# Performance work log

Hardware: AMD Instinct MI355X
Metric: run time of the kernel (lower is better)

## Reference

```python
import jax, jax.numpy as jnp
import numpy as np

B, E, H, C, R = 16, 1024, 1024, 64, 64  # batch, input_size, hidden_size, context_size, context_rank
H4 = 4 * H


def setup_inputs() -> dict:
    key = jax.random.key(0)
    ks = jax.random.split(key, 12)
    n = lambda k, shape, scale: jax.random.normal(k, shape, dtype=jnp.float32) * scale
    return {
        'x': n(ks[0], (B, E), 1.0),
        'h': n(ks[1], (B, H), 1.0),
        'c': n(ks[2], (B, H), 1.0),
        'context': n(ks[3], (B, C), 1.0),
        'Wi': n(ks[4], (E, H4), 0.02),
        'Wi_b': n(ks[5], (H4,), 0.02),
        'Wh': n(ks[6], (H, H4), 0.02),
        'Wh_b': n(ks[7], (H4,), 0.02),
        'AZ_il': n(ks[8], (C, E, R), 0.02),
        'AZ_ir': n(ks[9], (R, H4, C), 0.02),
        'AZ_hl': n(ks[10], (C, H, R), 0.02),
        'AZ_hr': n(ks[11], (R, H4, C), 0.02),
    }


def reference(x, h, c, context, Wi, Wi_b, Wh, Wh_b, AZ_il, AZ_ir, AZ_hl, AZ_hr):
    hs = Wh.shape[0]
    # compute_context_weights: per-sample low-rank weight perturbations
    lhs_i = jnp.einsum('bc,cer->ber', context, AZ_il)      # [B,E,R]
    rhs_i = jnp.einsum('bc,rjc->brj', context, AZ_ir)      # [B,R,4H]
    A_i = jnp.einsum('ber,brj->bej', lhs_i, rhs_i)         # [B,E,4H]
    lhs_h = jnp.einsum('bc,chr->bhr', context, AZ_hl)      # [B,H,R]
    rhs_h = jnp.einsum('bc,rjc->brj', context, AZ_hr)      # [B,R,4H]
    A_h = jnp.einsum('bhr,brj->bhj', lhs_h, rhs_h)         # [B,H,4H]
    # forward (faithful to original: context weights are multiplied by 0)
    Wi_eff = 0.0 * A_i + Wi                                # [B,E,4H]
    Wh_eff = 0.0 * A_h + Wh                                # [B,H,4H]
    ifgo = (jnp.einsum('be,bej->bj', x, Wi_eff) + Wi_b
            + jnp.einsum('bh,bhj->bj', h, Wh_eff) + Wh_b)  # [B,4H]
    i = jax.nn.sigmoid(ifgo[:, :hs])
    f = jax.nn.sigmoid(ifgo[:, hs:2 * hs])
    g = jnp.tanh(ifgo[:, 2 * hs:3 * hs])
    o = jax.nn.sigmoid(ifgo[:, 3 * hs:])
    c_new = f * c + i * g
    h_new = o * jnp.tanh(c_new)
    return (h_new, c_new)
```

## Files before the change

### kernel.cpp

```cpp
#include <hip/hip_runtime.h>
#include <stdint.h>

#define H4_ 4096
#define B_  16

__global__ __launch_bounds__(256) void k1_gemm(
    const float* __restrict__ x, const float* __restrict__ h,
    const float* __restrict__ Wi, const float* __restrict__ Wh,
    float* __restrict__ part)
{
    __shared__ float a_lds[256][16];
    __shared__ float red[8][16][32];

    const int s  = blockIdx.x & 7;
    const int ct = blockIdx.x >> 3;
    const int j0 = ct * 32;
    const int t  = threadIdx.x;
    const int c8 = t & 7;
    const int bq = (t >> 3) & 3;
    const int ks = t >> 5;

    float acc[4][4];
    #pragma unroll
    for (int r = 0; r < 4; r++)
        #pragma unroll
        for (int c = 0; c < 4; c++) acc[r][c] = 0.f;

    const float* A  = (s < 4) ? x : h;
    const float* W  = (s < 4) ? Wi : Wh;
    const int    e0 = (s & 3) * 256;

    {
        const int b = t & 15, kc = t >> 4;
        const float* src = A + b * 1024 + e0 + kc * 16;
        float4 v0 = *(const float4*)(src);
        float4 v1 = *(const float4*)(src + 4);
        float4 v2 = *(const float4*)(src + 8);
        float4 v3 = *(const float4*)(src + 12);
        const float vv[16] = { v0.x, v0.y, v0.z, v0.w, v1.x, v1.y, v1.z, v1.w,
                               v2.x, v2.y, v2.z, v2.w, v3.x, v3.y, v3.z, v3.w };
        #pragma unroll
        for (int j = 0; j < 16; j++) a_lds[kc * 16 + j][b] = vv[j];
    }
    __syncthreads();

    const float* wp = W + (size_t)e0 * H4_ + j0 + c8 * 4;
    #pragma unroll 8
    for (int i = 0; i < 32; i++) {
        const int kl = ks * 32 + i;
        float4 w = *(const float4*)(wp + (size_t)kl * H4_);
        float4 a = *(const float4*)&a_lds[kl][bq * 4];
        acc[0][0] += a.x * w.x; acc[0][1] += a.x * w.y; acc[0][2] += a.x * w.z; acc[0][3] += a.x * w.w;
        acc[1][0] += a.y * w.x; acc[1][1] += a.y * w.y; acc[1][2] += a.y * w.z; acc[1][3] += a.y * w.w;
        acc[2][0] += a.z * w.x; acc[2][1] += a.z * w.y; acc[2][2] += a.z * w.z; acc[2][3] += a.z * w.w;
        acc[3][0] += a.w * w.x; acc[3][1] += a.w * w.y; acc[3][2] += a.w * w.z; acc[3][3] += a.w * w.w;
    }

    #pragma unroll
    for (int r = 0; r < 4; r++)
        *(float4*)&red[ks][bq * 4 + r][c8 * 4] =
            make_float4(acc[r][0], acc[r][1], acc[r][2], acc[r][3]);
    __syncthreads();
    {
        const int b = t >> 4, c = t & 15;
        float s0 = 0.f, s1 = 0.f;
        #pragma unroll
        for (int kk = 0; kk < 8; kk++) {
            s0 += red[kk][b][c];
            s1 += red[kk][b][c + 16];
        }
        float* dst = part + ((size_t)s * B_ + b) * H4_ + j0;
        dst[c]      = s0;
        dst[c + 16] = s1;
    }
}

__global__ __launch_bounds__(256) void k2_act(
    const float* __restrict__ part, const float* __restrict__ c,
    const float* __restrict__ Wi_b, const float* __restrict__ Wh_b,
    float* __restrict__ out)
{
    const int tg = blockIdx.x * 256 + threadIdx.x;
    const int b  = tg >> 10;
    const int j  = tg & 1023;

    float g4[4];
    #pragma unroll
    for (int g = 0; g < 4; g++) {
        const int col = g * 1024 + j;
        float acc = Wi_b[col] + Wh_b[col];
        #pragma unroll
        for (int ss = 0; ss < 8; ss++)
            acc += part[((size_t)ss * B_ + b) * H4_ + col];
        g4[g] = acc;
    }
    const float ig = 1.f / (1.f + __expf(-g4[0]));
    const float fg = 1.f / (1.f + __expf(-g4[1]));
    const float gg = tanhf(g4[2]);
    const float og = 1.f / (1.f + __expf(-g4[3]));
    const float cv = c[tg];
    const float cn = fg * cv + ig * gg;
    const float hn = og * tanhf(cn);
    out[tg]         = hn;
    out[16384 + tg] = cn;
}

__global__ __launch_bounds__(256) void k_fused2(
    const float* __restrict__ x, const float* __restrict__ h,
    const float* __restrict__ cin,
    const float* __restrict__ Wi, const float* __restrict__ Wh,
    const float* __restrict__ Wi_b, const float* __restrict__ Wh_b,
    float* __restrict__ out)
{
    __shared__ float a_lds[256][16];
    __shared__ float red[16][16][16];
    __shared__ float gsum[16][16];

    const int bl = blockIdx.x;
    const int j0 = (bl & 7) * 128 + (bl >> 3) * 4;
    const int t  = threadIdx.x;
    const int g  = t & 3;
    const int bq = (t >> 2) & 3;
    const int ks = t >> 4;

    float acc[4][4];
    #pragma unroll
    for (int r = 0; r < 4; r++)
        #pragma unroll
        for (int c = 0; c < 4; c++) acc[r][c] = 0.f;

    for (int m = 0; m < 8; ++m) {
        const float* A  = (m < 4) ? x : h;
        const float* W  = (m < 4) ? Wi : Wh;
        const int    e0 = (m & 3) * 256;
        {
            const int b = t & 15, kc = t >> 4;
            const float* src = A + b * 1024 + e0 + kc * 16;
            float4 v0 = *(const float4*)(src);
            float4 v1 = *(const float4*)(src + 4);
            float4 v2 = *(const float4*)(src + 8);
            float4 v3 = *(const float4*)(src + 12);
            const float vv[16] = { v0.x, v0.y, v0.z, v0.w, v1.x, v1.y, v1.z, v1.w,
                                   v2.x, v2.y, v2.z, v2.w, v3.x, v3.y, v3.z, v3.w };
            #pragma unroll
            for (int jj = 0; jj < 16; jj++) a_lds[kc * 16 + jj][b] = vv[jj];
        }
        __syncthreads();
        const float* wp = W + (size_t)e0 * H4_ + g * 1024 + j0;
        #pragma unroll 4
        for (int i = 0; i < 16; i++) {
            const int kl = ks * 16 + i;
            float4 w = *(const float4*)(wp + (size_t)kl * H4_);
            float4 a = *(const float4*)&a_lds[kl][bq * 4];
            acc[0][0] += a.x * w.x; acc[0][1] += a.x * w.y; acc[0][2] += a.x * w.z; acc[0][3] += a.x * w.w;
            acc[1][0] += a.y * w.x; acc[1][1] += a.y * w.y; acc[1][2] += a.y * w.z; acc[1][3] += a.y * w.w;
            acc[2][0] += a.z * w.x; acc[2][1] += a.z * w.y; acc[2][2] += a.z * w.z; acc[2][3] += a.z * w.w;
            acc[3][0] += a.w * w.x; acc[3][1] += a.w * w.y; acc[3][2] += a.w * w.z; acc[3][3] += a.w * w.w;
        }
        __syncthreads();
    }

    #pragma unroll
    for (int r = 0; r < 4; r++)
        *(float4*)&red[ks][bq * 4 + r][g * 4] =
            make_float4(acc[r][0], acc[r][1], acc[r][2], acc[r][3]);
    __syncthreads();
    {
        const int b = t >> 4, c16 = t & 15;
        float sum = 0.f;
        #pragma unroll
        for (int kk = 0; kk < 16; kk++) sum += red[kk][b][c16];
        gsum[b][c16] = sum;
    }
    __syncthreads();

    if (t < 64) {
        const int b = t >> 2, jj = t & 3;
        const int j = j0 + jj;
        const float s0 = gsum[b][jj]      + Wi_b[j]        + Wh_b[j];
        const float s1 = gsum[b][4 + jj]  + Wi_b[1024 + j] + Wh_b[1024 + j];
        const float s2 = gsum[b][8 + jj]  + Wi_b[2048 + j] + Wh_b[2048 + j];
        const float s3 = gsum[b][12 + jj] + Wi_b[3072 + j] + Wh_b[3072 + j];
        const float ig = 1.f / (1.f + __expf(-s0));
        const float fg = 1.f / (1.f + __expf(-s1));
        const float gg = tanhf(s2);
        const float og = 1.f / (1.f + __expf(-s3));
        const float cv = cin[b * 1024 + j];
        const float cn = fg * cv + ig * gg;
        const float hn = og * tanhf(cn);
        out[b * 1024 + j]         = hn;
        out[16384 + b * 1024 + j] = cn;
    }
}

extern "C" void kernel_launch(void* const* d_in, const int* in_sizes, int n_in,
                              void* d_out, int out_size, void* d_ws, size_t ws_size,
                              hipStream_t stream) {
    (void)in_sizes; (void)n_in; (void)out_size;
    const float* x    = (const float*)d_in[0];
    const float* h    = (const float*)d_in[1];
    const float* c    = (const float*)d_in[2];
    const float* Wi   = (const float*)d_in[4];
    const float* Wi_b = (const float*)d_in[5];
    const float* Wh   = (const float*)d_in[6];
    const float* Wh_b = (const float*)d_in[7];

    float* part = (float*)d_ws;
    float* out  = (float*)d_out;

    const size_t need = 8ull * B_ * H4_ * sizeof(float);
    if (ws_size >= need) {
        k1_gemm<<<1024, 256, 0, stream>>>(x, h, Wi, Wh, part);
        k2_act<<<64, 256, 0, stream>>>(part, c, Wi_b, Wh_b, out);
    } else {
        k_fused2<<<64 * 4, 256, 0, stream>>>(x, h, c, Wi, Wh, Wi_b, Wh_b, out);
    }
}
```

Baseline: 182.9 us.

## Fuse split-K reduction and LSTM activation via last-block atomic ticket

```diff
diff --git a/kernel.cpp b/kernel.cpp
--- a/kernel.cpp
+++ b/kernel.cpp
@@ -4,31 +4,36 @@
 #define H4_ 4096
 #define B_  16
 
-__global__ __launch_bounds__(256) void k1_gemm(
+__global__ __launch_bounds__(256) void k1_fused(
     const float* __restrict__ x, const float* __restrict__ h,
+    const float* __restrict__ cin,
     const float* __restrict__ Wi, const float* __restrict__ Wh,
-    float* __restrict__ part)
+    const float* __restrict__ Wi_b, const float* __restrict__ Wh_b,
+    float* __restrict__ part, unsigned int* __restrict__ cnt,
+    float* __restrict__ out)
 {
     __shared__ float a_lds[256][16];
     __shared__ float red[8][16][32];
-
-    const int s  = blockIdx.x & 7;
-    const int ct = blockIdx.x >> 3;
+    __shared__ unsigned int ticket_s;
+
+    const int bl = blockIdx.x;
+    const int ct = bl & 127;
+    const int s  = bl >> 7;
     const int j0 = ct * 32;
     const int t  = threadIdx.x;
     const int c8 = t & 7;
     const int bq = (t >> 3) & 3;
     const int ks = t >> 5;
 
-    float acc[4][4];
-    #pragma unroll
-    for (int r = 0; r < 4; r++)
-        #pragma unroll
-        for (int c = 0; c < 4; c++) acc[r][c] = 0.f;
-
     const float* A  = (s < 4) ? x : h;
     const float* W  = (s < 4) ? Wi : Wh;
     const int    e0 = (s & 3) * 256;
+
+    float acc[4][4];
+    #pragma unroll
+    for (int r = 0; r < 4; r++)
+        #pragma unroll
+        for (int c = 0; c < 4; c++) acc[r][c] = 0.f;
 
     {
         const int b = t & 15, kc = t >> 4;
@@ -73,36 +78,40 @@
         dst[c]      = s0;
         dst[c + 16] = s1;
     }
-}
-
-__global__ __launch_bounds__(256) void k2_act(
-    const float* __restrict__ part, const float* __restrict__ c,
-    const float* __restrict__ Wi_b, const float* __restrict__ Wh_b,
-    float* __restrict__ out)
-{
-    const int tg = blockIdx.x * 256 + threadIdx.x;
-    const int b  = tg >> 10;
-    const int j  = tg & 1023;
-
-    float g4[4];
-    #pragma unroll
-    for (int g = 0; g < 4; g++) {
-        const int col = g * 1024 + j;
-        float acc = Wi_b[col] + Wh_b[col];
-        #pragma unroll
-        for (int ss = 0; ss < 8; ss++)
-            acc += part[((size_t)ss * B_ + b) * H4_ + col];
-        g4[g] = acc;
-    }
-    const float ig = 1.f / (1.f + __expf(-g4[0]));
-    const float fg = 1.f / (1.f + __expf(-g4[1]));
-    const float gg = tanhf(g4[2]);
-    const float og = 1.f / (1.f + __expf(-g4[3]));
-    const float cv = c[tg];
-    const float cn = fg * cv + ig * gg;
-    const float hn = og * tanhf(cn);
-    out[tg]         = hn;
-    out[16384 + tg] = cn;
+
+    __syncthreads();
+    if (t == 0)
+        ticket_s = __hip_atomic_fetch_add(&cnt[ct & 31], 1u,
+                       __ATOMIC_ACQ_REL, __HIP_MEMORY_SCOPE_AGENT);
+    __syncthreads();
+    if (ticket_s == 31) {
+        __threadfence();
+        const int w = ct & 31;
+        const int b = t >> 4, c = t & 15;
+        #pragma unroll
+        for (int half = 0; half < 2; ++half) {
+            const int j = w * 32 + c + half * 16;
+            float gs[4];
+            #pragma unroll
+            for (int g = 0; g < 4; g++) {
+                const int col = g * 1024 + j;
+                float a2 = Wi_b[col] + Wh_b[col];
+                #pragma unroll
+                for (int ss = 0; ss < 8; ss++)
+                    a2 += part[((size_t)ss * B_ + b) * H4_ + col];
+                gs[g] = a2;
+            }
+            const float ig = 1.f / (1.f + __expf(-gs[0]));
+            const float fg = 1.f / (1.f + __expf(-gs[1]));
+            const float gg = tanhf(gs[2]);
+            const float og = 1.f / (1.f + __expf(-gs[3]));
+            const float cv = cin[b * 1024 + j];
+            const float cn = fg * cv + ig * gg;
+            const float hn = og * tanhf(cn);
+            out[b * 1024 + j]         = hn;
+            out[16384 + b * 1024 + j] = cn;
+        }
+    }
 }
 
 __global__ __launch_bounds__(256) void k_fused2(
@@ -205,13 +214,17 @@
     const float* Wh   = (const float*)d_in[6];
     const float* Wh_b = (const float*)d_in[7];
 
-    float* part = (float*)d_ws;
-    float* out  = (float*)d_out;
-
-    const size_t need = 8ull * B_ * H4_ * sizeof(float);
-    if (ws_size >= need) {
-        k1_gemm<<<1024, 256, 0, stream>>>(x, h, Wi, Wh, part);
-        k2_act<<<64, 256, 0, stream>>>(part, c, Wi_b, Wh_b, out);
+    float* out = (float*)d_out;
+
+    const size_t part_bytes = 8ull * B_ * H4_ * sizeof(float);
+    const size_t cnt_bytes  = 32 * sizeof(unsigned int);
+
+    if (ws_size >= part_bytes + cnt_bytes) {
+        float* part        = (float*)d_ws;
+        unsigned int* cnt  = (unsigned int*)((char*)d_ws + part_bytes);
+        (void)hipMemsetAsync(cnt, 0, cnt_bytes, stream);
+        k1_fused<<<1024, 256, 0, stream>>>(x, h, c, Wi, Wh, Wi_b, Wh_b,
+                                           part, cnt, out);
     } else {
         k_fused2<<<64 * 4, 256, 0, stream>>>(x, h, c, Wi, Wh, Wi_b, Wh_b, out);
     }
```

New measurement: 227.2 us. 24.2% more time.
